# Optimization experiments

Measured on AMD Instinct MI355X. Metric: run time of the kernel, lower is better.

## Reference

```python
import jax, jax.numpy as jnp
import numpy as np
from jax import lax

IMG_SIZE = 640
STRIDES = (8, 16, 32)
NA = 3          # anchors per level
NC = 80         # classes
CONF_THRESH = 0.001
NMS_THRESH = 0.6
ANCHORS = np.array([[10,13],[16,30],[33,23],[30,61],[62,45],[59,119],[116,90],[156,198],[373,326]], np.float32).reshape(3, 3, 2)

def _make_grids():
    gs, st, aw = [], [], []
    for i, s in enumerate(STRIDES):
        hs = ws = IMG_SIZE // s
        gy, gx = np.meshgrid(np.arange(hs), np.arange(ws), indexing='ij')
        gxy = np.stack([gx, gy], -1).astype(np.float32).reshape(1, hs*ws, 1, 2)
        gs.append(gxy)
        st.append(np.full((1, hs*ws, NA, 2), s, np.float32))
        aw.append(np.tile(ANCHORS[i][None], (hs*ws, 1, 1)))
    return (np.concatenate(gs, 1), np.concatenate(st, 1), np.concatenate(aw, 0)[None])

GRID_CELL, STRIDE_T, ANCH_WH = _make_grids()  # [1,HW,1,2], [1,HW,3,2], [1,HW,3,2]

def _nms_classaware(boxes, score, valid):
    # Greedy NMS, class-aware via coordinate offset already applied to boxes.
    # Faithful to the numpy baseline: w,h = max(1e-28, .), areas without +1.
    x1, y1, x2, y2 = boxes[:, 0], boxes[:, 1], boxes[:, 2], boxes[:, 3]
    areas = (x2 - x1) * (y2 - y1)
    order = jnp.argsort(-score)
    N = boxes.shape[0]
    def body(i, state):
        supp, keep = state
        idx = order[i]
        active = jnp.logical_and(jnp.logical_not(supp[idx]), valid[idx])
        keep = keep.at[idx].set(active)
        xx1 = jnp.maximum(x1[idx], x1)
        yy1 = jnp.maximum(y1[idx], y1)
        xx2 = jnp.minimum(x2[idx], x2)
        yy2 = jnp.minimum(y2[idx], y2)
        w = jnp.maximum(1e-28, xx2 - xx1)
        h = jnp.maximum(1e-28, yy2 - yy1)
        inter = w * h
        iou = inter / (areas[idx] + areas - inter)
        newsupp = jnp.logical_and(iou > NMS_THRESH, active)
        newsupp = newsupp.at[idx].set(False)
        return jnp.logical_or(supp, newsupp), keep
    supp0 = jnp.zeros((N,), bool)
    keep0 = jnp.zeros((N,), bool)
    _, keep = lax.fori_loop(0, N, body, (supp0, keep0))
    return keep

def _decode_and_nms(pred_s, pred_m, pred_l):
    objs, clss, regs = [], [], []
    for pred in (pred_s, pred_m, pred_l):
        B, C, H, W = pred.shape
        p = pred.transpose(0, 2, 3, 1).reshape(B, H*W, C)
        objs.append(p[..., :NA].reshape(B, H*W*NA, 1))
        clss.append(p[..., NA:NA*(1+NC)].reshape(B, H*W*NA, NC))
        regs.append(p[..., NA*(1+NC):].reshape(B, H*W, NA, 4))
    obj_pred = jnp.concatenate(objs, axis=1)   # [B, N, 1]
    cls_pred = jnp.concatenate(clss, axis=1)   # [B, N, NC]
    reg_pred = jnp.concatenate(regs, axis=1)   # [B, HW, 3, 4]
    grid = jnp.asarray(GRID_CELL)
    stride = jnp.asarray(STRIDE_T)
    anch = jnp.asarray(ANCH_WH)
    B = reg_pred.shape[0]
    c_xy = (jax.nn.sigmoid(reg_pred[..., :2]) + grid) * stride
    b_wh = jnp.exp(reg_pred[..., 2:]) * anch
    xywh = jnp.concatenate([c_xy, b_wh], -1).reshape(B, -1, 4)
    x1y1 = xywh[..., :2] - xywh[..., 2:] / 2
    x2y2 = xywh[..., :2] + xywh[..., 2:] / 2
    boxes = jnp.clip(jnp.concatenate([x1y1, x2y2], -1) / IMG_SIZE, 0.0, 1.0)[0]  # [N,4]
    obj_s = jax.nn.sigmoid(obj_pred)[0]                     # [N,1]
    scores_all = jax.nn.softmax(cls_pred[0], axis=1) * obj_s  # [N,NC]
    cls_ind = jnp.argmax(scores_all, axis=1)                # [N]
    score = jnp.max(scores_all, axis=1)                     # [N]
    valid = score >= CONF_THRESH
    # class-aware NMS: offset normalized boxes by 2*class so classes never overlap
    boxes_off = boxes + cls_ind[:, None].astype(boxes.dtype) * 2.0
    keep = _nms_classaware(lax.stop_gradient(boxes_off), lax.stop_gradient(score), valid)
    out = jnp.concatenate([
        boxes,                                    # 4 cols
        score[:, None],                           # 1 col
        cls_ind[:, None].astype(boxes.dtype),     # 1 col (non-diff)
        keep[:, None].astype(boxes.dtype),        # 1 col (non-diff)
    ], axis=1)                                    # [N, 7]
    return out

def setup_inputs() -> dict:
    key = jax.random.key(0)
    k1, k2, k3 = jax.random.split(key, 3)
    return {
        'pred_s': jax.random.normal(k1, (1, 255, 80, 80), jnp.float32),
        'pred_m': jax.random.normal(k2, (1, 255, 40, 40), jnp.float32),
        'pred_l': jax.random.normal(k3, (1, 255, 20, 20), jnp.float32),
    }

def reference(pred_s, pred_m, pred_l):
    return _decode_and_nms(pred_s, pred_m, pred_l)
```

## Files before the change

### kernel.cpp

```cpp
#include <hip/hip_runtime.h>
#include <cstdint>

#define NPRED 25200
#define NPOS  8400
#define NCLS  80
#define CAP   512
#define CSTRIDE 16
#define MW    8

__device__ __forceinline__ float sigmoidf_(float x) { return 1.0f / (1.0f + expf(-x)); }

__global__ __launch_bounds__(64) void decode_kernel(
    const float* __restrict__ ps, const float* __restrict__ pm, const float* __restrict__ pl,
    float* __restrict__ out, int* __restrict__ counts, float* __restrict__ classbuf)
{
    int t = blockIdx.x * 64 + threadIdx.x;
    if (t >= NPRED) return;
    int a   = t / NPOS;
    int pos = t - a * NPOS;

    const float* p; int HW, W, base, si; float stride;
    if (pos < 6400)      { p = ps; HW = 6400; W = 80; stride = 8.f;  base = 0;    si = 0; }
    else if (pos < 8000) { p = pm; HW = 1600; W = 40; stride = 16.f; base = 6400; si = 1; }
    else                 { p = pl; HW = 400;  W = 20; stride = 32.f; base = 8000; si = 2; }
    int local = pos - base;
    int y = local / W;
    int x = local - y * W;

    const float AW[9] = {10.f,16.f,33.f, 30.f,62.f,59.f, 116.f,156.f,373.f};
    const float AH[9] = {13.f,30.f,23.f, 61.f,45.f,119.f, 90.f,198.f,326.f};
    float aw = AW[si*3 + a], ah = AH[si*3 + a];

    float objl = p[(size_t)a * HW + local];
    const float* rb = p + (size_t)(3 + 3 * NCLS + a * 4) * HW + local;
    float tx = rb[0], ty = rb[(size_t)HW], tw = rb[(size_t)2 * HW], th = rb[(size_t)3 * HW];

    const float* cb = p + (size_t)(3 + a * NCLS) * HW + local;
    float v[NCLS];
#pragma unroll
    for (int c = 0; c < NCLS; c++) v[c] = cb[(size_t)c * HW];

    float m = -INFINITY;
#pragma unroll
    for (int c = 0; c < NCLS; c++) m = fmaxf(m, v[c]);
    float s = 0.f;
#pragma unroll
    for (int c = 0; c < NCLS; c++) s += expf(v[c] - m);
    float obj = sigmoidf_(objl);
    float best = -1.f; int bi = 0;
#pragma unroll
    for (int c = 0; c < NCLS; c++) {
        float sc = expf(v[c] - m) / s * obj;
        if (sc > best) { best = sc; bi = c; }
    }

    float cx = (sigmoidf_(tx) + (float)x) * stride;
    float cy = (sigmoidf_(ty) + (float)y) * stride;
    float bw = expf(tw) * aw;
    float bh = expf(th) * ah;
    float x1 = fminf(fmaxf((cx - bw / 2.f) / 640.f, 0.f), 1.f);
    float y1 = fminf(fmaxf((cy - bh / 2.f) / 640.f, 0.f), 1.f);
    float x2 = fminf(fmaxf((cx + bw / 2.f) / 640.f, 0.f), 1.f);
    float y2 = fminf(fmaxf((cy + bh / 2.f) / 640.f, 0.f), 1.f);

    int g = pos * 3 + a;
    float clsf = (float)bi;
    float* o = out + (size_t)g * 7;
    o[0] = x1; o[1] = y1; o[2] = x2; o[3] = y2;
    o[4] = best; o[5] = clsf; o[6] = 0.f;

    if (best >= 0.001f) {
        int slot = atomicAdd(&counts[bi * CSTRIDE], 1);
        if (slot < CAP) {
            float off = clsf * 2.0f;
            float* r = classbuf + (size_t)(bi * CAP + slot) * 6;
            r[0] = x1 + off; r[1] = y1 + off; r[2] = x2 + off; r[3] = y2 + off;
            r[4] = best; r[5] = __int_as_float(g);
        }
    }
}

__global__ __launch_bounds__(256) void nms_sort_kernel(
    const int* __restrict__ counts, const float* __restrict__ classbuf,
    float4* __restrict__ g_sbox, int* __restrict__ g_sg)
{
    int c = blockIdx.x;
    int n = counts[c * CSTRIDE]; if (n > CAP) n = CAP;
    int tid = threadIdx.x;

    __shared__ uint64_t key[CAP];
    const float* cls = classbuf + (size_t)c * CAP * 6;

    for (int i = tid; i < n; i += 256) {
        unsigned u = __float_as_uint(cls[i * 6 + 4]);
        u = (u & 0x80000000u) ? ~u : (u | 0x80000000u);
        key[i] = ((uint64_t)(~u) << 15) | (uint64_t)__float_as_int(cls[i * 6 + 5]);
    }
    __syncthreads();

    for (int i = tid; i < n; i += 256) {
        uint64_t k = key[i];
        int r = 0;
        for (int j = 0; j < n; j++) r += (key[j] < k);
        g_sbox[c * CAP + r] = make_float4(cls[i * 6 + 0], cls[i * 6 + 1],
                                          cls[i * 6 + 2], cls[i * 6 + 3]);
        g_sg[c * CAP + r] = (int)(k & 0x7FFF);
    }
}

__global__ __launch_bounds__(256) void nms_build_kernel(
    const int* __restrict__ counts, const float4* __restrict__ g_sbox,
    uint64_t* __restrict__ g_mask)
{
    int c = blockIdx.x;
    int w = blockIdx.y;
    int n = counts[c * CSTRIDE]; if (n > CAP) n = CAP;
    int j0 = w << 6;
    if (j0 >= n) return;
    int j1 = j0 + 64; if (j1 > n) j1 = n;
    int cnt = j1 - j0;
    int tid = threadIdx.x;

    __shared__ float4 sb[64];
    if (tid < cnt) sb[tid] = g_sbox[c * CAP + j0 + tid];
    __syncthreads();

    uint64_t* gm = g_mask + (size_t)c * MW * CAP + (size_t)w * CAP;
    for (int i = tid; i < n; i += 256) {
        float4 b4 = g_sbox[c * CAP + i];
        float Ai = (b4.z - b4.x) * (b4.w - b4.y);
        uint64_t bits = 0;
        if (i + 1 < j1) {
            for (int j = 0; j < cnt; j++) {
                float4 bj = sb[j];
                float xx1 = fmaxf(b4.x, bj.x);
                float yy1 = fmaxf(b4.y, bj.y);
                float xx2 = fminf(b4.z, bj.z);
                float yy2 = fminf(b4.w, bj.w);
                float ww = fmaxf(1e-28f, xx2 - xx1);
                float hh = fmaxf(1e-28f, yy2 - yy1);
                float inter = ww * hh;
                float Aj = (bj.z - bj.x) * (bj.w - bj.y);
                float iou = inter / ((Ai + Aj) - inter);
                if ((j0 + j) > i && iou > 0.6f) bits |= 1ull << j;
            }
        }
        gm[i] = bits;
    }
}

__global__ __launch_bounds__(64) void nms_scan_kernel(
    const int* __restrict__ counts, const int* __restrict__ g_sg,
    const uint64_t* __restrict__ g_mask, float* __restrict__ out)
{
    int c = blockIdx.x;
    int n = counts[c * CSTRIDE]; if (n > CAP) n = CAP;
    int nw = (n + 63) >> 6;
    int lane = threadIdx.x;

    const uint64_t* gm = g_mask + (size_t)c * MW * CAP;
    const int* sg = g_sg + c * CAP;

    uint64_t removed = 0;
    for (int w = 0; w < nw; w++) {
        uint64_t rw = __shfl(removed, w);
        int row = (w << 6) + lane;
        uint64_t diag = (row < n) ? gm[w * CAP + row] : 0ull;
        int rem = n - (w << 6);
        uint64_t valid = (rem >= 64) ? ~0ull : ((1ull << rem) - 1ull);
        uint64_t nulls = __ballot(diag == 0ull);
        uint64_t cand = ~rw & valid;
        uint64_t kw = 0;
        uint64_t it = cand & ~nulls;
        while (it) {
            int b = __ffsll((unsigned long long)it) - 1;
            kw |= 1ull << b;
            uint64_t db = __shfl(diag, b);
            it &= ~db; cand &= ~db;
            it &= ~(1ull << b);
        }
        kw |= cand & nulls;

        int g  = lane >> 3;
        int wp = lane & 7;
        uint64_t acc = 0;
        if (wp < nw) {
            uint64_t mybits = kw & (0xFFull << (g * 8));
            while (mybits) {
                int b = __ffsll((unsigned long long)mybits) - 1;
                mybits &= mybits - 1;
                acc |= gm[wp * CAP + ((w << 6) + b)];
            }
        }
        acc |= __shfl_xor(acc, 8);
        acc |= __shfl_xor(acc, 16);
        acc |= __shfl_xor(acc, 32);
        if (lane < MW) removed |= acc;

        if (row < n && ((kw >> lane) & 1))
            out[(size_t)sg[row] * 7 + 6] = 1.0f;
    }
}

extern "C" void kernel_launch(void* const* d_in, const int* in_sizes, int n_in,
                              void* d_out, int out_size, void* d_ws, size_t ws_size,
                              hipStream_t stream) {
    const float* ps = (const float*)d_in[0];
    const float* pm = (const float*)d_in[1];
    const float* pl = (const float*)d_in[2];
    float* out = (float*)d_out;

    char* ws = (char*)d_ws;
    int*      counts   = (int*)ws;
    float*    classbuf = (float*)(ws + 8192);
    int*      g_sg     = (int*)(ws + 8192 + 983040);
    float4*   g_sbox   = (float4*)(ws + 8192 + 983040 + 163840);
    uint64_t* g_mask   = (uint64_t*)(ws + 8192 + 983040 + 163840 + 655360);

    hipMemsetAsync(counts, 0, 8192, stream);
    decode_kernel<<<(NPRED + 63) / 64, 64, 0, stream>>>(ps, pm, pl, out, counts, classbuf);
    nms_sort_kernel<<<NCLS, 256, 0, stream>>>(counts, classbuf, g_sbox, g_sg);
    nms_build_kernel<<<dim3(NCLS, MW), 256, 0, stream>>>(counts, g_sbox, g_mask);
    nms_scan_kernel<<<NCLS, 64, 0, stream>>>(counts, g_sg, g_mask, out);
}
```

Before: 115.1 us.

## Stage class logits through LDS with float4 loads in decode kernel

The decode kernel now uses a 2D grid of (spatial chunk, anchor) blocks. Each block cooperatively loads the 80 class rows for its 64 positions as float4 vectors into shared memory, then computes softmax and argmax from LDS. The exps are cached in LDS so they are not recomputed in the argmax pass. This replaces per-thread scalar strided loads and an 80-float register array, which should ease register pressure and improve load width. The cost is added LDS traffic and a barrier. Edge chunks clamp their offsets, so some lanes load duplicate data.

```diff
diff --git a/kernel.cpp b/kernel.cpp
--- a/kernel.cpp
+++ b/kernel.cpp
@@ -7,6 +7,7 @@
 #define CAP   512
 #define CSTRIDE 16
 #define MW    8
+#define NCHUNK 132
 
 __device__ __forceinline__ float sigmoidf_(float x) { return 1.0f / (1.0f + expf(-x)); }
 
@@ -14,46 +15,63 @@
     const float* __restrict__ ps, const float* __restrict__ pm, const float* __restrict__ pl,
     float* __restrict__ out, int* __restrict__ counts, float* __restrict__ classbuf)
 {
-    int t = blockIdx.x * 64 + threadIdx.x;
-    if (t >= NPRED) return;
-    int a   = t / NPOS;
-    int pos = t - a * NPOS;
-
-    const float* p; int HW, W, base, si; float stride;
-    if (pos < 6400)      { p = ps; HW = 6400; W = 80; stride = 8.f;  base = 0;    si = 0; }
-    else if (pos < 8000) { p = pm; HW = 1600; W = 40; stride = 16.f; base = 6400; si = 1; }
-    else                 { p = pl; HW = 400;  W = 20; stride = 32.f; base = 8000; si = 2; }
-    int local = pos - base;
-    int y = local / W;
-    int x = local - y * W;
+    int chunk = blockIdx.x;
+    int a     = blockIdx.y;
+    int t     = threadIdx.x;
+
+    const float* p; int HW, W, base, si; float stride; int w0;
+    if (chunk < 100)      { p = ps; HW = 6400; W = 80; stride = 8.f;  base = 0;    si = 0; w0 = chunk * 64; }
+    else if (chunk < 125) { p = pm; HW = 1600; W = 40; stride = 16.f; base = 6400; si = 1; w0 = (chunk - 100) * 64; }
+    else                  { p = pl; HW = 400;  W = 20; stride = 32.f; base = 8000; si = 2; w0 = (chunk - 125) * 64; }
+
+    int local = w0 + t;
+    bool valid = local < HW;
+    int lclamp = valid ? local : (HW - 1);
+
+    __shared__ float lds[NCLS * 64];
+
+    const float* cbase = p + (size_t)(3 + a * NCLS) * HW;
+    int lane_c = t >> 4;
+    int j      = (t & 15) << 2;
+    int off    = w0 + j; if (off > HW - 4) off = HW - 4;
+#pragma unroll
+    for (int r0 = 0; r0 < NCLS; r0 += 4) {
+        int c = r0 + lane_c;
+        float4 v4 = *(const float4*)(cbase + (size_t)c * HW + off);
+        *(float4*)&lds[c * 64 + j] = v4;
+    }
+
+    float objl = p[(size_t)a * HW + lclamp];
+    const float* rb = p + (size_t)(3 + 3 * NCLS + a * 4) * HW + lclamp;
+    float tx = rb[0], ty = rb[(size_t)HW], tw = rb[(size_t)2 * HW], th = rb[(size_t)3 * HW];
+    __syncthreads();
+
+    float m = -INFINITY;
+#pragma unroll 16
+    for (int c = 0; c < NCLS; c++) m = fmaxf(m, lds[c * 64 + t]);
+    float s = 0.f;
+#pragma unroll 16
+    for (int c = 0; c < NCLS; c++) {
+        float e = expf(lds[c * 64 + t] - m);
+        lds[c * 64 + t] = e;
+        s += e;
+    }
+    float obj = sigmoidf_(objl);
+    float best = -1.f; int bi = 0;
+#pragma unroll 16
+    for (int c = 0; c < NCLS; c++) {
+        float sc = lds[c * 64 + t] / s * obj;
+        if (sc > best) { best = sc; bi = c; }
+    }
+
+    if (!valid) return;
 
     const float AW[9] = {10.f,16.f,33.f, 30.f,62.f,59.f, 116.f,156.f,373.f};
     const float AH[9] = {13.f,30.f,23.f, 61.f,45.f,119.f, 90.f,198.f,326.f};
     float aw = AW[si*3 + a], ah = AH[si*3 + a];
 
-    float objl = p[(size_t)a * HW + local];
-    const float* rb = p + (size_t)(3 + 3 * NCLS + a * 4) * HW + local;
-    float tx = rb[0], ty = rb[(size_t)HW], tw = rb[(size_t)2 * HW], th = rb[(size_t)3 * HW];
-
-    const float* cb = p + (size_t)(3 + a * NCLS) * HW + local;
-    float v[NCLS];
-#pragma unroll
-    for (int c = 0; c < NCLS; c++) v[c] = cb[(size_t)c * HW];
-
-    float m = -INFINITY;
-#pragma unroll
-    for (int c = 0; c < NCLS; c++) m = fmaxf(m, v[c]);
-    float s = 0.f;
-#pragma unroll
-    for (int c = 0; c < NCLS; c++) s += expf(v[c] - m);
-    float obj = sigmoidf_(objl);
-    float best = -1.f; int bi = 0;
-#pragma unroll
-    for (int c = 0; c < NCLS; c++) {
-        float sc = expf(v[c] - m) / s * obj;
-        if (sc > best) { best = sc; bi = c; }
-    }
-
+    int y = local / W;
+    int x = local - y * W;
     float cx = (sigmoidf_(tx) + (float)x) * stride;
     float cy = (sigmoidf_(ty) + (float)y) * stride;
     float bw = expf(tw) * aw;
@@ -63,7 +81,7 @@
     float x2 = fminf(fmaxf((cx + bw / 2.f) / 640.f, 0.f), 1.f);
     float y2 = fminf(fmaxf((cy + bh / 2.f) / 640.f, 0.f), 1.f);
 
-    int g = pos * 3 + a;
+    int g = (base + local) * 3 + a;
     float clsf = (float)bi;
     float* o = out + (size_t)g * 7;
     o[0] = x1; o[1] = y1; o[2] = x2; o[3] = y2;
@@ -72,9 +90,9 @@
     if (best >= 0.001f) {
         int slot = atomicAdd(&counts[bi * CSTRIDE], 1);
         if (slot < CAP) {
-            float off = clsf * 2.0f;
+            float off2 = clsf * 2.0f;
             float* r = classbuf + (size_t)(bi * CAP + slot) * 6;
-            r[0] = x1 + off; r[1] = y1 + off; r[2] = x2 + off; r[3] = y2 + off;
+            r[0] = x1 + off2; r[1] = y1 + off2; r[2] = x2 + off2; r[3] = y2 + off2;
             r[4] = best; r[5] = __int_as_float(g);
         }
     }
@@ -218,7 +236,7 @@
     uint64_t* g_mask   = (uint64_t*)(ws + 8192 + 983040 + 163840 + 655360);
 
     hipMemsetAsync(counts, 0, 8192, stream);
-    decode_kernel<<<(NPRED + 63) / 64, 64, 0, stream>>>(ps, pm, pl, out, counts, classbuf);
+    decode_kernel<<<dim3(NCHUNK, 3), 64, 0, stream>>>(ps, pm, pl, out, counts, classbuf);
     nms_sort_kernel<<<NCLS, 256, 0, stream>>>(counts, classbuf, g_sbox, g_sg);
     nms_build_kernel<<<dim3(NCLS, MW), 256, 0, stream>>>(counts, g_sbox, g_mask);
     nms_scan_kernel<<<NCLS, 64, 0, stream>>>(counts, g_sg, g_mask, out);
```

New measurement: 119.4 us. 1.04x slower.
